# Optimization experiments

Measured on AMD Instinct MI355X. Metric: run time of the kernel, lower is better.

## Reference

```python
import jax, jax.numpy as jnp
import numpy as np

N_NODES = 50000
N_EDGES = 800000
IN_DIM = 128
HID = 64
HEADS = 2
OUT_DIM = 2
N_GRAPHS = 512
NEG_SLOPE = 0.2


def setup_inputs() -> dict:
    key = jax.random.key(0)
    ks = jax.random.split(key, 16)
    x = jax.random.normal(ks[0], (N_NODES, IN_DIM), dtype=jnp.float32)
    edge_index = jax.random.randint(ks[1], (2, N_EDGES), 0, N_NODES, dtype=jnp.int64)
    batch = jnp.sort(jax.random.randint(ks[2], (N_NODES,), 0, N_GRAPHS, dtype=jnp.int64))
    s = 0.1
    W1 = jax.random.normal(ks[3], (IN_DIM, HEADS * HID), dtype=jnp.float32) * s
    a_src1 = jax.random.normal(ks[4], (HEADS, HID), dtype=jnp.float32) * s
    a_dst1 = jax.random.normal(ks[5], (HEADS, HID), dtype=jnp.float32) * s
    b1 = jnp.zeros((HEADS * HID,), dtype=jnp.float32)
    W2 = jax.random.normal(ks[6], (HEADS * HID, HID), dtype=jnp.float32) * s
    a_src2 = jax.random.normal(ks[7], (1, HID), dtype=jnp.float32) * s
    a_dst2 = jax.random.normal(ks[8], (1, HID), dtype=jnp.float32) * s
    b2 = jnp.zeros((HID,), dtype=jnp.float32)
    fcW = jax.random.normal(ks[9], (HID, OUT_DIM), dtype=jnp.float32) * s
    fcb = jnp.zeros((OUT_DIM,), dtype=jnp.float32)
    return dict(x=x, edge_index=edge_index, batch=batch,
                W1=W1, a_src1=a_src1, a_dst1=a_dst1, b1=b1,
                W2=W2, a_src2=a_src2, a_dst2=a_dst2, b2=b2,
                fcW=fcW, fcb=fcb)


def gat_layer(x, src, dst, W, a_src, a_dst, b, heads, c_out):
    # x: [N, F] -> h: [N, H, C]
    N = x.shape[0]
    h = (x @ W).reshape(N, heads, c_out)
    alpha_s = jnp.sum(h * a_src, axis=-1)  # [N, H]
    alpha_d = jnp.sum(h * a_dst, axis=-1)  # [N, H]
    e = jax.nn.leaky_relu(alpha_s[src] + alpha_d[dst], NEG_SLOPE)  # [E, H]
    # segment softmax over destination nodes
    emax = jax.ops.segment_max(e, dst, num_segments=N)  # [N, H]
    ex = jnp.exp(e - emax[dst])
    denom = jax.ops.segment_sum(ex, dst, num_segments=N)  # [N, H]
    coef = ex / denom[dst]  # [E, H]
    msg = h[src] * coef[..., None]  # [E, H, C]
    out = jax.ops.segment_sum(msg, dst, num_segments=N)  # [N, H, C]
    return out.reshape(N, heads * c_out) + b


def reference(x, edge_index, batch, W1, a_src1, a_dst1, b1, W2, a_src2, a_dst2, b2, fcW, fcb):
    N = x.shape[0]
    # PyG GATConv add_self_loops=True (shared graph for both layers)
    loops = jnp.arange(N, dtype=edge_index.dtype)
    src = jnp.concatenate([edge_index[0], loops])
    dst = jnp.concatenate([edge_index[1], loops])
    h = jax.nn.relu(gat_layer(x, src, dst, W1, a_src1, a_dst1, b1, HEADS, HID))
    h = jax.nn.relu(gat_layer(h, src, dst, W2, a_src2, a_dst2, b2, 1, HID))
    # global mean pool over graphs
    sums = jax.ops.segment_sum(h, batch, num_segments=N_GRAPHS)  # [G, HID]
    cnts = jax.ops.segment_sum(jnp.ones((N,), dtype=h.dtype), batch, num_segments=N_GRAPHS)
    pooled = sums / jnp.maximum(cnts, 1.0)[:, None]
    logits = pooled @ fcW + fcb
    return jax.nn.log_softmax(logits, axis=1)
```

## Files before the change

### kernel.cpp

```cpp
#include <hip/hip_runtime.h>
#include <math.h>

#define N_NODES 50000
#define N_EDGES 800000
#define EP (N_EDGES + N_NODES)
#define IN_DIM 128
#define HID 64
#define HEADS 2
#define OUT_DIM 2
#define N_GRAPHS 512
#define NEG_SLOPE 0.2f
#define NB_SCAN 196
#define GA_GEMM 782
#define GB_GEMM 781
#define GB_BASE 25024
#define G_HIST 3321
#define G_SCAT 3321

typedef unsigned int uint;
typedef unsigned short ushort;

__device__ __forceinline__ ushort f2bf(float f) {
    uint u = __float_as_uint(f);
    u += 0x7fffu + ((u >> 16) & 1u);
    return (ushort)(u >> 16);
}
__device__ __forceinline__ float bf_lo(uint u) { return __uint_as_float(u << 16); }
__device__ __forceinline__ float bf_hi(uint u) { return __uint_as_float(u & 0xffff0000u); }
__device__ __forceinline__ float lrelu(float e) { return e > 0.f ? e : NEG_SLOPE * e; }

__device__ __forceinline__ void gemm1_block(float (*xs)[128], int base_block,
                                            const float* __restrict__ X,
                                            const float* __restrict__ W,
                                            ushort* __restrict__ Y,
                                            const float* __restrict__ a_src,
                                            const float* __restrict__ a_dst,
                                            float* __restrict__ as, float* __restrict__ ad) {
    const int wave = threadIdx.x >> 6;
    const int lane = threadIdx.x & 63;
    const int base = base_block + wave * 8;
    const float4* X4 = (const float4*)X;
    for (int idx = lane; idx < 8 * 32; idx += 64) {
        int r = idx >> 5, c = idx & 31;
        int n = base + r;
        float4 v = (n < N_NODES) ? X4[(size_t)n * 32 + c] : make_float4(0.f, 0.f, 0.f, 0.f);
        ((float4*)xs[wave * 8 + r])[c] = v;
    }
    __syncthreads();

    float acc0[8], acc1[8];
#pragma unroll
    for (int i = 0; i < 8; i++) { acc0[i] = 0.f; acc1[i] = 0.f; }
    for (int k = 0; k < 128; k += 4) {
        float wA[4], wB[4];
#pragma unroll
        for (int kk = 0; kk < 4; kk++) {
            wA[kk] = W[(size_t)(k + kk) * 128 + lane];
            wB[kk] = W[(size_t)(k + kk) * 128 + 64 + lane];
        }
#pragma unroll
        for (int i = 0; i < 8; i++) {
            float4 xv = *(const float4*)&xs[wave * 8 + i][k];
            acc0[i] = fmaf(xv.x, wA[0], acc0[i]); acc1[i] = fmaf(xv.x, wB[0], acc1[i]);
            acc0[i] = fmaf(xv.y, wA[1], acc0[i]); acc1[i] = fmaf(xv.y, wB[1], acc1[i]);
            acc0[i] = fmaf(xv.z, wA[2], acc0[i]); acc1[i] = fmaf(xv.z, wB[2], acc1[i]);
            acc0[i] = fmaf(xv.w, wA[3], acc0[i]); acc1[i] = fmaf(xv.w, wB[3], acc1[i]);
        }
    }

    const float asv0 = a_src[lane],      adv0 = a_dst[lane];
    const float asv1 = a_src[64 + lane], adv1 = a_dst[64 + lane];
#pragma unroll
    for (int i = 0; i < 8; i++) {
        int n = base + i;
        if (n >= N_NODES) continue;
        Y[(size_t)n * 128 + lane]      = f2bf(acc0[i]);
        Y[(size_t)n * 128 + 64 + lane] = f2bf(acc1[i]);
        float s0 = acc0[i] * asv0, d0 = acc0[i] * adv0;
        float s1 = acc1[i] * asv1, d1 = acc1[i] * adv1;
#pragma unroll
        for (int off = 32; off; off >>= 1) {
            s0 += __shfl_xor(s0, off);
            d0 += __shfl_xor(d0, off);
            s1 += __shfl_xor(s1, off);
            d1 += __shfl_xor(d1, off);
        }
        if (lane == 0) {
            as[(size_t)n * 2 + 0] = s0; as[(size_t)n * 2 + 1] = s1;
            ad[(size_t)n * 2 + 0] = d0; ad[(size_t)n * 2 + 1] = d1;
        }
    }
}

__global__ void fused_gemm1a_hist(const float* __restrict__ X, const float* __restrict__ W,
                                  ushort* __restrict__ Y,
                                  const float* __restrict__ a_src, const float* __restrict__ a_dst,
                                  float* __restrict__ as, float* __restrict__ ad,
                                  const int* __restrict__ ei, int* __restrict__ cnt,
                                  int* __restrict__ erank) {
    __shared__ float xs[32][128];
    if (blockIdx.x >= GA_GEMM) {
        int i = (blockIdx.x - GA_GEMM) * 256 + threadIdx.x;
        if (i < EP) {
            int d = (i < N_EDGES) ? ei[N_EDGES + i] : (i - N_EDGES);
            erank[i] = atomicAdd(&cnt[d], 1);
        }
        return;
    }
    gemm1_block(xs, blockIdx.x * 32, X, W, Y, a_src, a_dst, as, ad);
}

__global__ void fused_gemm1b_scatter(const float* __restrict__ X, const float* __restrict__ W,
                                     ushort* __restrict__ Y,
                                     const float* __restrict__ a_src, const float* __restrict__ a_dst,
                                     float* __restrict__ as, float* __restrict__ ad,
                                     const int* __restrict__ ei, const int* __restrict__ rowptr,
                                     const int* __restrict__ erank, int* __restrict__ csr_src) {
    __shared__ float xs[32][128];
    if (blockIdx.x >= GB_GEMM) {
        int i = (blockIdx.x - GB_GEMM) * 256 + threadIdx.x;
        if (i < EP) {
            int s, d;
            if (i < N_EDGES) { s = ei[i]; d = ei[N_EDGES + i]; }
            else             { s = d = i - N_EDGES; }
            csr_src[rowptr[d] + erank[i]] = s;
        }
        return;
    }
    gemm1_block(xs, GB_BASE + blockIdx.x * 32, X, W, Y, a_src, a_dst, as, ad);
}

__global__ void partial_kernel(const int* __restrict__ cnt, int* __restrict__ bsum) {
    int tid = threadIdx.x;
    int i = blockIdx.x * 256 + tid;
    int lane = tid & 63, wid = tid >> 6;
    int v = (i < N_NODES) ? cnt[i] : 0;
#pragma unroll
    for (int off = 32; off; off >>= 1) v += __shfl_xor(v, off);
    __shared__ int wsum[4];
    if (lane == 0) wsum[wid] = v;
    __syncthreads();
    if (tid == 0) bsum[blockIdx.x] = wsum[0] + wsum[1] + wsum[2] + wsum[3];
}

__global__ void scanc_kernel(const int* __restrict__ cnt, const int* __restrict__ bsum,
                             int* __restrict__ rowptr) {
    int tid = threadIdx.x;
    int lane = tid & 63, wid = tid >> 6;
    __shared__ int wtA[4], wtB[4];
    __shared__ int s_boff;

    int bv = (tid < NB_SCAN) ? bsum[tid] : 0;
    int bincl = bv;
#pragma unroll
    for (int off = 1; off < 64; off <<= 1) {
        int t = __shfl_up(bincl, off);
        if (lane >= off) bincl += t;
    }
    if (lane == 63) wtA[wid] = bincl;
    __syncthreads();
    int addA = 0;
    for (int w = 0; w < wid; w++) addA += wtA[w];
    bincl += addA;
    if (tid == blockIdx.x) s_boff = bincl - bv;
    if (blockIdx.x == 0 && tid == NB_SCAN - 1) rowptr[N_NODES] = bincl;

    int i = blockIdx.x * 256 + tid;
    int v = (i < N_NODES) ? cnt[i] : 0;
    int incl = v;
#pragma unroll
    for (int off = 1; off < 64; off <<= 1) {
        int t = __shfl_up(incl, off);
        if (lane >= off) incl += t;
    }
    if (lane == 63) wtB[wid] = incl;
    __syncthreads();
    int add = s_boff;
    for (int w = 0; w < wid; w++) add += wtB[w];
    if (i < N_NODES) rowptr[i] = add + incl - v;
}

__global__ void gemm_alphas2(const float* __restrict__ X, const float* __restrict__ W,
                             ushort* __restrict__ Y,
                             const float* __restrict__ a_src, const float* __restrict__ a_dst,
                             float* __restrict__ as, float* __restrict__ ad, int n_nodes) {
    __shared__ float xs[8][128];
    const int base = blockIdx.x * 8;
    const int t = threadIdx.x;
    const int g = t >> 5, c = t & 31;
    const float4* X4 = (const float4*)X;
    for (int idx = t; idx < 8 * 32; idx += 64) {
        int r = idx >> 5, cc = idx & 31;
        int n = base + r;
        float4 v = (n < n_nodes) ? X4[(size_t)n * 32 + cc] : make_float4(0.f, 0.f, 0.f, 0.f);
        ((float4*)xs[r])[cc] = v;
    }
    __syncthreads();

    float acc0[4], acc1[4];
#pragma unroll
    for (int i = 0; i < 4; i++) { acc0[i] = 0.f; acc1[i] = 0.f; }
    for (int k = 0; k < 128; k += 4) {
        float wA[4], wB[4];
#pragma unroll
        for (int kk = 0; kk < 4; kk++) {
            wA[kk] = W[(size_t)(k + kk) * 64 + c];
            wB[kk] = W[(size_t)(k + kk) * 64 + 32 + c];
        }
#pragma unroll
        for (int i = 0; i < 4; i++) {
            float4 xv = *(const float4*)&xs[g * 4 + i][k];
            acc0[i] = fmaf(xv.x, wA[0], acc0[i]); acc1[i] = fmaf(xv.x, wB[0], acc1[i]);
            acc0[i] = fmaf(xv.y, wA[1], acc0[i]); acc1[i] = fmaf(xv.y, wB[1], acc1[i]);
            acc0[i] = fmaf(xv.z, wA[2], acc0[i]); acc1[i] = fmaf(xv.z, wB[2], acc1[i]);
            acc0[i] = fmaf(xv.w, wA[3], acc0[i]); acc1[i] = fmaf(xv.w, wB[3], acc1[i]);
        }
    }

    const float asvA = a_src[c], asvB = a_src[32 + c];
    const float advA = a_dst[c], advB = a_dst[32 + c];
#pragma unroll
    for (int i = 0; i < 4; i++) {
        int n = base + g * 4 + i;
        if (n >= n_nodes) continue;
        Y[(size_t)n * 64 + c]      = f2bf(acc0[i]);
        Y[(size_t)n * 64 + 32 + c] = f2bf(acc1[i]);
        float s = acc0[i] * asvA + acc1[i] * asvB;
        float d = acc0[i] * advA + acc1[i] * advB;
#pragma unroll
        for (int off = 16; off; off >>= 1) {
            s += __shfl_xor(s, off);
            d += __shfl_xor(d, off);
        }
        if (c == 0) { as[n] = s; ad[n] = d; }
    }
}

__global__ void node_agg1_kernel(const int* __restrict__ rowptr, const int* __restrict__ csr_src,
                                 const uint* __restrict__ Hb,
                                 const float* __restrict__ as, const float* __restrict__ ad,
                                 const float* __restrict__ b, float* __restrict__ outp) {
    int wave = threadIdx.x >> 6;
    int lane = threadIdx.x & 63;
    int node = blockIdx.x * 4 + wave;
    if (node >= N_NODES) return;
    const int lo = rowptr[node], hi = rowptr[node + 1];
    const float ad0 = ad[(size_t)node * 2 + 0], ad1 = ad[(size_t)node * 2 + 1];

    float exa0 = 0.f, exa1 = 0.f, exb0 = 0.f, exb1 = 0.f;
    int j1 = lo + lane;
    if (j1 < hi) {
        int s = csr_src[j1];
        float2 a = *(const float2*)&as[(size_t)s * 2];
        exa0 = __expf(lrelu(a.x + ad0));
        exa1 = __expf(lrelu(a.y + ad1));
    }
    int j2 = lo + 64 + lane;
    if (j2 < hi) {
        int s = csr_src[j2];
        float2 a = *(const float2*)&as[(size_t)s * 2];
        exb0 = __expf(lrelu(a.x + ad0));
        exb1 = __expf(lrelu(a.y + ad1));
    }
    float d0 = exa0 + exb0, d1 = exa1 + exb1;
    for (int j = lo + 128 + lane; j < hi; j += 64) {
        int s = csr_src[j];
        float2 a = *(const float2*)&as[(size_t)s * 2];
        d0 += __expf(lrelu(a.x + ad0));
        d1 += __expf(lrelu(a.y + ad1));
    }
#pragma unroll
    for (int off = 32; off; off >>= 1) {
        d0 += __shfl_xor(d0, off);
        d1 += __shfl_xor(d1, off);
    }
    const float inv = (lane < 32) ? (1.f / d0) : (1.f / d1);
    const bool h0side = (lane < 32);

    float acc0 = 0.f, acc1 = 0.f;
    const int deg = hi - lo;
    const int n1 = deg < 64 ? deg : 64;
    int j = 0;
    for (; j + 8 <= n1; j += 8) {
        int s0 = csr_src[lo + j + 0], s1 = csr_src[lo + j + 1];
        int s2 = csr_src[lo + j + 2], s3 = csr_src[lo + j + 3];
        int s4 = csr_src[lo + j + 4], s5 = csr_src[lo + j + 5];
        int s6 = csr_src[lo + j + 6], s7 = csr_src[lo + j + 7];
        uint u0 = Hb[(size_t)s0 * 64 + lane];
        uint u1 = Hb[(size_t)s1 * 64 + lane];
        uint u2 = Hb[(size_t)s2 * 64 + lane];
        uint u3 = Hb[(size_t)s3 * 64 + lane];
        uint u4 = Hb[(size_t)s4 * 64 + lane];
        uint u5 = Hb[(size_t)s5 * 64 + lane];
        uint u6 = Hb[(size_t)s6 * 64 + lane];
        uint u7 = Hb[(size_t)s7 * 64 + lane];
        float ca0 = __shfl(exa0, j + 0), cb0 = __shfl(exa1, j + 0);
        float ca1 = __shfl(exa0, j + 1), cb1 = __shfl(exa1, j + 1);
        float ca2 = __shfl(exa0, j + 2), cb2 = __shfl(exa1, j + 2);
        float ca3 = __shfl(exa0, j + 3), cb3 = __shfl(exa1, j + 3);
        float ca4 = __shfl(exa0, j + 4), cb4 = __shfl(exa1, j + 4);
        float ca5 = __shfl(exa0, j + 5), cb5 = __shfl(exa1, j + 5);
        float ca6 = __shfl(exa0, j + 6), cb6 = __shfl(exa1, j + 6);
        float ca7 = __shfl(exa0, j + 7), cb7 = __shfl(exa1, j + 7);
        float c0 = h0side ? ca0 : cb0;
        float c1 = h0side ? ca1 : cb1;
        float c2 = h0side ? ca2 : cb2;
        float c3 = h0side ? ca3 : cb3;
        float c4 = h0side ? ca4 : cb4;
        float c5 = h0side ? ca5 : cb5;
        float c6 = h0side ? ca6 : cb6;
        float c7 = h0side ? ca7 : cb7;
        acc0 = fmaf(bf_lo(u0), c0, acc0); acc1 = fmaf(bf_hi(u0), c0, acc1);
        acc0 = fmaf(bf_lo(u1), c1, acc0); acc1 = fmaf(bf_hi(u1), c1, acc1);
        acc0 = fmaf(bf_lo(u2), c2, acc0); acc1 = fmaf(bf_hi(u2), c2, acc1);
        acc0 = fmaf(bf_lo(u3), c3, acc0); acc1 = fmaf(bf_hi(u3), c3, acc1);
        acc0 = fmaf(bf_lo(u4), c4, acc0); acc1 = fmaf(bf_hi(u4), c4, acc1);
        acc0 = fmaf(bf_lo(u5), c5, acc0); acc1 = fmaf(bf_hi(u5), c5, acc1);
        acc0 = fmaf(bf_lo(u6), c6, acc0); acc1 = fmaf(bf_hi(u6), c6, acc1);
        acc0 = fmaf(bf_lo(u7), c7, acc0); acc1 = fmaf(bf_hi(u7), c7, acc1);
    }
    for (; j < n1; j++) {
        int s = csr_src[lo + j];
        float ca = __shfl(exa0, j), cb = __shfl(exa1, j);
        float c = h0side ? ca : cb;
        uint u = Hb[(size_t)s * 64 + lane];
        acc0 = fmaf(bf_lo(u), c, acc0);
        acc1 = fmaf(bf_hi(u), c, acc1);
    }
    if (deg > 64) {
        const int n2 = deg < 128 ? deg : 128;
        for (j = 64; j < n2; j++) {
            int s = csr_src[lo + j];
            float ca = __shfl(exb0, j - 64), cb = __shfl(exb1, j - 64);
            float c = h0side ? ca : cb;
            uint u = Hb[(size_t)s * 64 + lane];
            acc0 = fmaf(bf_lo(u), c, acc0);
            acc1 = fmaf(bf_hi(u), c, acc1);
        }
        for (int jj = lo + 128; jj < hi; jj++) {
            int s = csr_src[jj];
            float2 a = *(const float2*)&as[(size_t)s * 2];
            float e0 = __expf(lrelu(a.x + ad0));
            float e1 = __expf(lrelu(a.y + ad1));
            float c = h0side ? e0 : e1;
            uint u = Hb[(size_t)s * 64 + lane];
            acc0 = fmaf(bf_lo(u), c, acc0);
            acc1 = fmaf(bf_hi(u), c, acc1);
        }
    }
    float v0 = acc0 * inv + b[2 * lane];
    float v1 = acc1 * inv + b[2 * lane + 1];
    v0 = v0 > 0.f ? v0 : 0.f;
    v1 = v1 > 0.f ? v1 : 0.f;
    *(float2*)&outp[(size_t)node * 128 + 2 * lane] = make_float2(v0, v1);
}

__global__ void node_agg2_kernel(const int* __restrict__ rowptr, const int* __restrict__ csr_src,
                                 const ushort* __restrict__ Hb,
                                 const float* __restrict__ as, const float* __restrict__ ad,
                                 const float* __restrict__ b, float* __restrict__ outp) {
    int wave = threadIdx.x >> 6;
    int lane = threadIdx.x & 63;
    int node = blockIdx.x * 4 + wave;
    if (node >= N_NODES) return;
    const int lo = rowptr[node], hi = rowptr[node + 1];
    const float adN = ad[node];

    float exa = 0.f, exb = 0.f;
    int j1 = lo + lane;
    if (j1 < hi) exa = __expf(lrelu(as[csr_src[j1]] + adN));
    int j2 = lo + 64 + lane;
    if (j2 < hi) exb = __expf(lrelu(as[csr_src[j2]] + adN));
    float d = exa + exb;
    for (int j = lo + 128 + lane; j < hi; j += 64)
        d += __expf(lrelu(as[csr_src[j]] + adN));
#pragma unroll
    for (int off = 32; off; off >>= 1) d += __shfl_xor(d, off);
    const float inv = 1.f / d;

    float acc = 0.f;
    const int deg = hi - lo;
    const int n1 = deg < 64 ? deg : 64;
    int j = 0;
    for (; j + 8 <= n1; j += 8) {
        int s0 = csr_src[lo + j + 0], s1 = csr_src[lo + j + 1];
        int s2 = csr_src[lo + j + 2], s3 = csr_src[lo + j + 3];
        int s4 = csr_src[lo + j + 4], s5 = csr_src[lo + j + 5];
        int s6 = csr_src[lo + j + 6], s7 = csr_src[lo + j + 7];
        float h0 = __uint_as_float(((uint)Hb[(size_t)s0 * 64 + lane]) << 16);
        float h1 = __uint_as_float(((uint)Hb[(size_t)s1 * 64 + lane]) << 16);
        float h2 = __uint_as_float(((uint)Hb[(size_t)s2 * 64 + lane]) << 16);
        float h3 = __uint_as_float(((uint)Hb[(size_t)s3 * 64 + lane]) << 16);
        float h4 = __uint_as_float(((uint)Hb[(size_t)s4 * 64 + lane]) << 16);
        float h5 = __uint_as_float(((uint)Hb[(size_t)s5 * 64 + lane]) << 16);
        float h6 = __uint_as_float(((uint)Hb[(size_t)s6 * 64 + lane]) << 16);
        float h7 = __uint_as_float(((uint)Hb[(size_t)s7 * 64 + lane]) << 16);
        float c0 = __shfl(exa, j + 0), c1 = __shfl(exa, j + 1);
        float c2 = __shfl(exa, j + 2), c3 = __shfl(exa, j + 3);
        float c4 = __shfl(exa, j + 4), c5 = __shfl(exa, j + 5);
        float c6 = __shfl(exa, j + 6), c7 = __shfl(exa, j + 7);
        acc = fmaf(h0, c0, acc);
        acc = fmaf(h1, c1, acc);
        acc = fmaf(h2, c2, acc);
        acc = fmaf(h3, c3, acc);
        acc = fmaf(h4, c4, acc);
        acc = fmaf(h5, c5, acc);
        acc = fmaf(h6, c6, acc);
        acc = fmaf(h7, c7, acc);
    }
    for (; j < n1; j++) {
        float c = __shfl(exa, j);
        acc = fmaf(__uint_as_float(((uint)Hb[(size_t)csr_src[lo + j] * 64 + lane]) << 16), c, acc);
    }
    if (deg > 64) {
        const int n2 = deg < 128 ? deg : 128;
        for (j = 64; j < n2; j++) {
            float c = __shfl(exb, j - 64);
            acc = fmaf(__uint_as_float(((uint)Hb[(size_t)csr_src[lo + j] * 64 + lane]) << 16), c, acc);
        }
        for (int jj = lo + 128; jj < hi; jj++) {
            int s = csr_src[jj];
            float c = __expf(lrelu(as[s] + adN));
            acc = fmaf(__uint_as_float(((uint)Hb[(size_t)s * 64 + lane]) << 16), c, acc);
        }
    }
    float v = acc * inv + b[lane];
    outp[(size_t)node * 64 + lane] = v > 0.f ? v : 0.f;
}

__global__ void pool_fc_kernel(const float* __restrict__ act2,
                               const int* __restrict__ batch,
                               const float* __restrict__ fcW,
                               const float* __restrict__ fcb,
                               float* __restrict__ out) {
    int g = blockIdx.x;
    int tid = threadIdx.x;
    int wid = tid >> 6, c = tid & 63;
    __shared__ int slo, shi;
    if (tid == 0) {
        int lo = 0, hi = N_NODES;
        while (lo < hi) { int m = (lo + hi) >> 1; if (batch[m] < g) lo = m + 1; else hi = m; }
        slo = lo;
        lo = 0; hi = N_NODES;
        while (lo < hi) { int m = (lo + hi) >> 1; if (batch[m] < g + 1) lo = m + 1; else hi = m; }
        shi = lo;
    }
    __syncthreads();
    const int lo = slo, hi = shi;
    float sum = 0.f;
    for (int n = lo + wid; n < hi; n += 4) sum += act2[(size_t)n * HID + c];
    __shared__ float ps[4][HID];
    ps[wid][c] = sum;
    __syncthreads();
    if (wid == 0) {
        float t = ps[0][c] + ps[1][c] + ps[2][c] + ps[3][c];
        float cnt = (float)(hi - lo);
        __shared__ float pooled[HID];
        pooled[c] = t / fmaxf(cnt, 1.f);
        __syncthreads();
        __shared__ float ls[OUT_DIM];
        if (c < OUT_DIM) {
            float l = fcb[c];
#pragma unroll 8
            for (int k = 0; k < HID; k++) l = fmaf(pooled[k], fcW[k * OUT_DIM + c], l);
            ls[c] = l;
        }
        __syncthreads();
        if (c < OUT_DIM) {
            float m = fmaxf(ls[0], ls[1]);
            float lse = m + logf(expf(ls[0] - m) + expf(ls[1] - m));
            out[(size_t)g * OUT_DIM + c] = ls[c] - lse;
        }
    }
}

extern "C" void kernel_launch(void* const* d_in, const int* in_sizes, int n_in,
                              void* d_out, int out_size, void* d_ws, size_t ws_size,
                              hipStream_t stream) {
    const float* x    = (const float*)d_in[0];
    const int*   ei   = (const int*)d_in[1];
    const int*   batch= (const int*)d_in[2];
    const float* W1   = (const float*)d_in[3];
    const float* as1w = (const float*)d_in[4];
    const float* ad1w = (const float*)d_in[5];
    const float* b1   = (const float*)d_in[6];
    const float* W2   = (const float*)d_in[7];
    const float* as2w = (const float*)d_in[8];
    const float* ad2w = (const float*)d_in[9];
    const float* b2   = (const float*)d_in[10];
    const float* fcW  = (const float*)d_in[11];
    const float* fcb  = (const float*)d_in[12];

    const size_t N = N_NODES;
    float* ws = (float*)d_ws;
    ushort* h1b  = (ushort*)ws;
    float* act1  = ws + N * 64;
    ushort* h2b  = (ushort*)(act1 + N * 128);
    float* out2  = act1 + N * 128 + N * 32;
    float* alps1 = out2 + N * 64;
    float* alpd1 = alps1 + N * 2;
    float* alps2 = alpd1 + N * 2;
    float* alpd2 = alps2 + N;
    int* cnt     = (int*)(alpd2 + N);
    int* rowptr  = cnt + N;
    int* bsum    = rowptr + N + 1;
    int* erank   = bsum + NB_SCAN;
    int* csr_src = erank + EP;

    hipMemsetAsync(cnt, 0, N * sizeof(int), stream);
    fused_gemm1a_hist<<<GA_GEMM + G_HIST, 256, 0, stream>>>(
        x, W1, h1b, as1w, ad1w, alps1, alpd1, ei, cnt, erank);

    partial_kernel<<<NB_SCAN, 256, 0, stream>>>(cnt, bsum);
    scanc_kernel<<<NB_SCAN, 256, 0, stream>>>(cnt, bsum, rowptr);

    fused_gemm1b_scatter<<<GB_GEMM + G_SCAT, 256, 0, stream>>>(
        x, W1, h1b, as1w, ad1w, alps1, alpd1, ei, rowptr, erank, csr_src);

    node_agg1_kernel<<<(N + 3) / 4, 256, 0, stream>>>(
        rowptr, csr_src, (const uint*)h1b, alps1, alpd1, b1, act1);

    gemm_alphas2<<<(N + 7) / 8, 64, 0, stream>>>(
        act1, W2, h2b, as2w, ad2w, alps2, alpd2, (int)N);
    node_agg2_kernel<<<(N + 3) / 4, 256, 0, stream>>>(
        rowptr, csr_src, h2b, alps2, alpd2, b2, out2);

    pool_fc_kernel<<<N_GRAPHS, 256, 0, stream>>>(out2, batch, fcW, fcb, (float*)d_out);
}
```

Measured before the change: 307.1 us.

## Replace random CSR scatter with two-pass bucketed scatter via shared memory

```diff
diff --git a/kernel.cpp b/kernel.cpp
--- a/kernel.cpp
+++ b/kernel.cpp
@@ -1,5 +1,6 @@
 #include <hip/hip_runtime.h>
 #include <math.h>
+#include <stdint.h>
 
 #define N_NODES 50000
 #define N_EDGES 800000
@@ -11,11 +12,9 @@
 #define N_GRAPHS 512
 #define NEG_SLOPE 0.2f
 #define NB_SCAN 196
-#define GA_GEMM 782
-#define GB_GEMM 781
-#define GB_BASE 25024
+#define G_GEMM1 1563
 #define G_HIST 3321
-#define G_SCAT 3321
+#define NBKT 208
 
 typedef unsigned int uint;
 typedef unsigned short ushort;
@@ -29,16 +28,24 @@
 __device__ __forceinline__ float bf_hi(uint u) { return __uint_as_float(u & 0xffff0000u); }
 __device__ __forceinline__ float lrelu(float e) { return e > 0.f ? e : NEG_SLOPE * e; }
 
-__device__ __forceinline__ void gemm1_block(float (*xs)[128], int base_block,
-                                            const float* __restrict__ X,
-                                            const float* __restrict__ W,
-                                            ushort* __restrict__ Y,
-                                            const float* __restrict__ a_src,
-                                            const float* __restrict__ a_dst,
-                                            float* __restrict__ as, float* __restrict__ ad) {
+__global__ void fused_gemm1_hist(const float* __restrict__ X, const float* __restrict__ W,
+                                 ushort* __restrict__ Y,
+                                 const float* __restrict__ a_src, const float* __restrict__ a_dst,
+                                 float* __restrict__ as, float* __restrict__ ad,
+                                 const int* __restrict__ ei, int* __restrict__ cnt,
+                                 int* __restrict__ erank) {
+    if (blockIdx.x >= G_GEMM1) {
+        int i = (blockIdx.x - G_GEMM1) * 256 + threadIdx.x;
+        if (i < EP) {
+            int d = (i < N_EDGES) ? ei[N_EDGES + i] : (i - N_EDGES);
+            erank[i] = atomicAdd(&cnt[d], 1);
+        }
+        return;
+    }
+    __shared__ float xs[32][128];
     const int wave = threadIdx.x >> 6;
     const int lane = threadIdx.x & 63;
-    const int base = base_block + wave * 8;
+    const int base = blockIdx.x * 32 + wave * 8;
     const float4* X4 = (const float4*)X;
     for (int idx = lane; idx < 8 * 32; idx += 64) {
         int r = idx >> 5, c = idx & 31;
@@ -92,46 +99,10 @@
     }
 }
 
-__global__ void fused_gemm1a_hist(const float* __restrict__ X, const float* __restrict__ W,
-                                  ushort* __restrict__ Y,
-                                  const float* __restrict__ a_src, const float* __restrict__ a_dst,
-                                  float* __restrict__ as, float* __restrict__ ad,
-                                  const int* __restrict__ ei, int* __restrict__ cnt,
-                                  int* __restrict__ erank) {
-    __shared__ float xs[32][128];
-    if (blockIdx.x >= GA_GEMM) {
-        int i = (blockIdx.x - GA_GEMM) * 256 + threadIdx.x;
-        if (i < EP) {
-            int d = (i < N_EDGES) ? ei[N_EDGES + i] : (i - N_EDGES);
-            erank[i] = atomicAdd(&cnt[d], 1);
-        }
-        return;
-    }
-    gemm1_block(xs, blockIdx.x * 32, X, W, Y, a_src, a_dst, as, ad);
-}
-
-__global__ void fused_gemm1b_scatter(const float* __restrict__ X, const float* __restrict__ W,
-                                     ushort* __restrict__ Y,
-                                     const float* __restrict__ a_src, const float* __restrict__ a_dst,
-                                     float* __restrict__ as, float* __restrict__ ad,
-                                     const int* __restrict__ ei, const int* __restrict__ rowptr,
-                                     const int* __restrict__ erank, int* __restrict__ csr_src) {
-    __shared__ float xs[32][128];
-    if (blockIdx.x >= GB_GEMM) {
-        int i = (blockIdx.x - GB_GEMM) * 256 + threadIdx.x;
-        if (i < EP) {
-            int s, d;
-            if (i < N_EDGES) { s = ei[i]; d = ei[N_EDGES + i]; }
-            else             { s = d = i - N_EDGES; }
-            csr_src[rowptr[d] + erank[i]] = s;
-        }
-        return;
-    }
-    gemm1_block(xs, GB_BASE + blockIdx.x * 32, X, W, Y, a_src, a_dst, as, ad);
-}
-
-__global__ void partial_kernel(const int* __restrict__ cnt, int* __restrict__ bsum) {
+__global__ void partial_kernel(const int* __restrict__ cnt, int* __restrict__ bsum,
+                               int* __restrict__ gcursor) {
     int tid = threadIdx.x;
+    if (blockIdx.x == 0 && tid < NBKT) gcursor[tid] = tid * 4096;
     int i = blockIdx.x * 256 + tid;
     int lane = tid & 63, wid = tid >> 6;
     int v = (i < N_NODES) ? cnt[i] : 0;
@@ -178,6 +149,61 @@
     int add = s_boff;
     for (int w = 0; w < wid; w++) add += wtB[w];
     if (i < N_NODES) rowptr[i] = add + incl - v;
+}
+
+__global__ void bucketA_kernel(const int* __restrict__ ei, const int* __restrict__ rowptr,
+                               const int* __restrict__ erank, int* __restrict__ gcursor,
+                               int2* __restrict__ pairbuf) {
+    __shared__ int bcnt[NBKT];
+    __shared__ int bbase[NBKT];
+    const int tid = threadIdx.x;
+    for (int b = tid; b < NBKT; b += 256) bcnt[b] = 0;
+    __syncthreads();
+    int pos[16], sv[16];
+    const int base_i = blockIdx.x * 4096;
+#pragma unroll
+    for (int k = 0; k < 16; k++) {
+        int i = base_i + k * 256 + tid;
+        pos[k] = -1;
+        if (i < EP) {
+            int s, d;
+            if (i < N_EDGES) { s = ei[i]; d = ei[N_EDGES + i]; }
+            else             { s = d = i - N_EDGES; }
+            int p = rowptr[d] + erank[i];
+            pos[k] = p; sv[k] = s;
+            atomicAdd(&bcnt[p >> 12], 1);
+        }
+    }
+    __syncthreads();
+    for (int b = tid; b < NBKT; b += 256) {
+        int c = bcnt[b];
+        bbase[b] = (c > 0) ? atomicAdd(&gcursor[b], c) : 0;
+    }
+    __syncthreads();
+    for (int b = tid; b < NBKT; b += 256) bcnt[b] = 0;
+    __syncthreads();
+#pragma unroll
+    for (int k = 0; k < 16; k++) {
+        if (pos[k] >= 0) {
+            int b = pos[k] >> 12;
+            int r = atomicAdd(&bcnt[b], 1);
+            pairbuf[bbase[b] + r] = make_int2(pos[k], sv[k]);
+        }
+    }
+}
+
+__global__ void bucketB_kernel(const int2* __restrict__ pairbuf, int* __restrict__ csr_src) {
+    __shared__ int sbuf[4096];
+    const int tid = threadIdx.x;
+    const int base = blockIdx.x * 4096;
+    const int cnt = (EP - base < 4096) ? (EP - base) : 4096;
+    for (int j = tid; j < cnt; j += 256) {
+        int2 pr = pairbuf[base + j];
+        sbuf[pr.x - base] = pr.y;
+    }
+    __syncthreads();
+    for (int j = tid; j < cnt; j += 256)
+        csr_src[base + j] = sbuf[j];
 }
 
 __global__ void gemm_alphas2(const float* __restrict__ X, const float* __restrict__ W,
@@ -504,18 +530,20 @@
     int* cnt     = (int*)(alpd2 + N);
     int* rowptr  = cnt + N;
     int* bsum    = rowptr + N + 1;
-    int* erank   = bsum + NB_SCAN;
+    int* gcursor = bsum + NB_SCAN;
+    int* erank   = gcursor + NBKT;
     int* csr_src = erank + EP;
+    int2* pairbuf = (int2*)(((uintptr_t)(csr_src + EP) + 7) & ~(uintptr_t)7);
 
     hipMemsetAsync(cnt, 0, N * sizeof(int), stream);
-    fused_gemm1a_hist<<<GA_GEMM + G_HIST, 256, 0, stream>>>(
+    fused_gemm1_hist<<<G_GEMM1 + G_HIST, 256, 0, stream>>>(
         x, W1, h1b, as1w, ad1w, alps1, alpd1, ei, cnt, erank);
 
-    partial_kernel<<<NB_SCAN, 256, 0, stream>>>(cnt, bsum);
+    partial_kernel<<<NB_SCAN, 256, 0, stream>>>(cnt, bsum, gcursor);
     scanc_kernel<<<NB_SCAN, 256, 0, stream>>>(cnt, bsum, rowptr);
 
-    fused_gemm1b_scatter<<<GB_GEMM + G_SCAT, 256, 0, stream>>>(
-        x, W1, h1b, as1w, ad1w, alps1, alpd1, ei, rowptr, erank, csr_src);
+    bucketA_kernel<<<NBKT, 256, 0, stream>>>(ei, rowptr, erank, gcursor, pairbuf);
+    bucketB_kernel<<<NBKT, 256, 0, stream>>>(pairbuf, csr_src);
 
     node_agg1_kernel<<<(N + 3) / 4, 256, 0, stream>>>(
         rowptr, csr_src, (const uint*)h1b, alps1, alpd1, b1, act1);
```

After: 303.6 us. No clear change (-1.1%).
